# Kernel optimization log

Measured on AMD Instinct MI355X. Metric: run time of the kernel, lower is better.

Reference implementation:

```python
import jax, jax.numpy as jnp
import numpy as np

NHEAD = 16
NEG1 = -9e15   # first masked_fill value (-9000000000000000.0)
NEG2 = -9e16   # second masked_fill value


def setup_inputs() -> dict:
    key = jax.random.key(0)
    ks = jax.random.split(key, 8)
    slen, bsz, emb = 512, 16, 1024
    x = jax.random.normal(ks[0], (slen, bsz, emb), dtype=jnp.float32)
    mask = jax.random.randint(ks[1], (bsz, slen, slen), 0, 2, dtype=jnp.int32)
    weight_mask = jax.random.randint(ks[2], (bsz, slen, slen), 0, 2, dtype=jnp.int32)
    s = 1.0 / np.sqrt(emb)
    Wq = jax.random.normal(ks[3], (emb, emb), dtype=jnp.float32) * s
    Wk = jax.random.normal(ks[4], (emb, emb), dtype=jnp.float32) * s
    Wv = jax.random.normal(ks[5], (emb, emb), dtype=jnp.float32) * s
    Ws = jax.random.normal(ks[6], (emb, emb), dtype=jnp.float32) * s
    Wb = jax.random.normal(ks[7], (1, 3 * emb), dtype=jnp.float32) * s
    return {"x": x, "mask": mask, "weight_mask": weight_mask,
            "Wq": Wq, "Wk": Wk, "Wv": Wv, "Ws": Ws, "Wb": Wb}


def reference(x, mask, weight_mask, Wq, Wk, Wv, Ws, Wb):
    slen, bsz, emb = x.shape
    hd = emb // NHEAD
    scaling = float(hd) ** -0.5

    def split_heads(t):  # (slen, bsz, emb) -> (bsz, nhead, slen, hd)
        return t.reshape(slen, bsz, NHEAD, hd).transpose(1, 2, 0, 3)

    q = split_heads(x @ Wq.T)
    k = split_heads(x @ Wk.T)
    v = split_heads(x @ Wv.T)

    attn = jnp.einsum('bhqd,bhkd->bhqk', q, k) * scaling

    m = mask.astype(attn.dtype)[:, None, :, :]          # (bsz,1,slen,slen)
    attn = jnp.where(m == 0, NEG1, attn)
    attn = jax.nn.softmax(attn, axis=-1) * m

    wm = weight_mask.astype(attn.dtype)[:, None, :, :]
    attn = jnp.where(wm == 0, NEG2, attn)
    attn = jax.nn.softmax(attn, axis=-1) * wm
    # degree normalization: row-normalize
    attn = attn * (1.0 / (attn.sum(-1) + 1e-10))[..., None]

    # dropout inactive (eval mode)
    out = jnp.einsum('bhqk,bhkd->bhqd', attn, v)         # (bsz,nhead,slen,hd)
    out = out.transpose(2, 0, 1, 3).reshape(slen, bsz, emb)

    r = x @ Ws.T
    gate = jax.nn.sigmoid(jnp.concatenate([out, r, out - r], axis=-1) @ Wb.T)
    return gate * r + (1.0 - gate) * out
```

## Files before the change

kernel.cpp:

```cpp
#include <hip/hip_runtime.h>
#include <hip/hip_bf16.h>
#include <stdint.h>

typedef __attribute__((ext_vector_type(8))) short short8;
typedef __attribute__((ext_vector_type(4))) float f32x4;
typedef __attribute__((ext_vector_type(4))) unsigned short ushort4v;

#define MFMA_BF16(a,b,c) __builtin_amdgcn_mfma_f32_16x16x32_bf16((a),(b),(c),0,0,0)

static __device__ __forceinline__ unsigned short f2bf(float f){
  union { float fv; unsigned int u; } c; c.fv = f;
  unsigned int u = c.u;
  return (unsigned short)((u + 0x7fffu + ((u >> 16) & 1u)) >> 16);
}

static __device__ __forceinline__ unsigned int cvtpk(float a, float b){
  unsigned int r;
  asm("v_cvt_pk_bf16_f32 %0, %1, %2" : "=v"(r) : "v"(a), "v"(b));
  return r;
}

static __device__ __forceinline__ void gload_lds16(const void* g, void* l){
  __builtin_amdgcn_global_load_lds(
      (const __attribute__((address_space(1))) void*)g,
      (__attribute__((address_space(3))) void*)l, 16, 0, 0);
}

static __device__ __forceinline__ float wred_sum(float v){
  #pragma unroll
  for (int m = 32; m; m >>= 1) v += __shfl_xor(v, m, 64);
  return v;
}

static __device__ __forceinline__ void unpack8(uint4 u, float* f){
  f[0] = __uint_as_float(u.x << 16); f[1] = __uint_as_float(u.x & 0xFFFF0000u);
  f[2] = __uint_as_float(u.y << 16); f[3] = __uint_as_float(u.y & 0xFFFF0000u);
  f[4] = __uint_as_float(u.z << 16); f[5] = __uint_as_float(u.z & 0xFFFF0000u);
  f[6] = __uint_as_float(u.w << 16); f[7] = __uint_as_float(u.w & 0xFFFF0000u);
}

__global__ __launch_bounds__(256) void cvt_x_kernel(const float* __restrict__ x,
                                                    unsigned short* __restrict__ o){
  int i = blockIdx.x * 256 + threadIdx.x;
  float4 f = ((const float4*)x)[i];
  ushort4v r;
  r[0] = f2bf(f.x); r[1] = f2bf(f.y); r[2] = f2bf(f.z); r[3] = f2bf(f.w);
  ((ushort4v*)o)[i] = r;
}

__global__ __launch_bounds__(256) void cvt_w_kernel(const float* __restrict__ Wq,
                                                    const float* __restrict__ Wk,
                                                    const float* __restrict__ Wv,
                                                    const float* __restrict__ Ws,
                                                    unsigned short* __restrict__ B){
  int i = blockIdx.x * 256 + threadIdx.x;
  int which = i >> 18;
  const float* src = (which == 0) ? Wq : (which == 1) ? Wk : (which == 2) ? Wv : Ws;
  float4 f = ((const float4*)src)[i & 262143];
  ushort4v r;
  r[0] = f2bf(f.x); r[1] = f2bf(f.y); r[2] = f2bf(f.z); r[3] = f2bf(f.w);
  ((ushort4v*)B)[i] = r;
}

__global__ void wb_prep_kernel(const float* __restrict__ Wb,
                               float* __restrict__ wba, float* __restrict__ wbb){
  int e = blockIdx.x * 256 + threadIdx.x;
  if (e < 1024){
    wba[e] = Wb[e]        + Wb[2048 + e];
    wbb[e] = Wb[1024 + e] - Wb[2048 + e];
  }
}

__global__ __launch_bounds__(256) void mask_prep_kernel(
    const int* __restrict__ m, const int* __restrict__ wm,
    unsigned long long* __restrict__ mb, unsigned long long* __restrict__ wb)
{
  const size_t i = (size_t)blockIdx.x * 256 + threadIdx.x;
  const int a = m[i];
  const int c = wm[i];
  unsigned long long ba = __ballot(a != 0);
  unsigned long long bc = __ballot(c != 0);
  if ((threadIdx.x & 63) == 0){
    mb[i >> 6] = ba;
    wb[i >> 6] = bc;
  }
}

__global__ __launch_bounds__(256, 4) void gemm_proj_kernel(
    const unsigned short* __restrict__ X, const unsigned short* __restrict__ B,
    unsigned short* __restrict__ qb, unsigned short* __restrict__ kb,
    unsigned short* __restrict__ vT, unsigned short* __restrict__ rbb)
{
  __shared__ __align__(16) unsigned short smem[128 * 136];
  unsigned short* As = smem;
  unsigned short* Bs = smem + 4096;
  const int tid = threadIdx.x;
  const int w = tid >> 6, l = tid & 63;
  const int lr = l & 15, lq = l >> 4;
  const int wr = w >> 1, wc = w & 1;
  const int bid = ((blockIdx.x & 7) << 8) | (blockIdx.x >> 3);
  const int m0 = (bid >> 5) * 128;
  const int n0 = (bid & 31) * 128;
  const int gsw = (lr >> 1) & 3;
  f32x4 acc[4][4] = {};

  for (int k0 = 0; k0 < 1024; k0 += 32){
    #pragma unroll
    for (int i = 0; i < 2; i++){
      const int c = i * 256 + tid;
      const int row = c >> 2;
      const int cgs = (c & 3) ^ ((c >> 3) & 3);
      gload_lds16(X + (size_t)(m0 + row) * 1024 + k0 + cgs * 8,
                  As + (i * 256 + w * 64) * 8);
      gload_lds16(B + (size_t)(n0 + row) * 1024 + k0 + cgs * 8,
                  Bs + (i * 256 + w * 64) * 8);
    }
    __syncthreads();
    short8 av[4], bv[4];
    #pragma unroll
    for (int mf = 0; mf < 4; mf++)
      av[mf] = *(const short8*)(As + (wr * 64 + mf * 16 + lr) * 32 + (lq ^ gsw) * 8);
    #pragma unroll
    for (int nf = 0; nf < 4; nf++)
      bv[nf] = *(const short8*)(Bs + (wc * 64 + nf * 16 + lr) * 32 + (lq ^ gsw) * 8);
    #pragma unroll
    for (int mf = 0; mf < 4; mf++)
      #pragma unroll
      for (int nf = 0; nf < 4; nf++)
        acc[mf][nf] = MFMA_BF16(av[mf], bv[nf], acc[mf][nf]);
    __syncthreads();
  }

  const int which = (n0 >> 10);
  const int o0 = n0 & 1023;
  if (which == 2){
    #pragma unroll
    for (int mf = 0; mf < 4; mf++)
      #pragma unroll
      for (int nf = 0; nf < 4; nf++){
        const int r0 = wr * 64 + mf * 16 + lq * 4;
        const int c  = wc * 64 + nf * 16 + lr;
        uint2 pk;
        pk.x = cvtpk(acc[mf][nf][0], acc[mf][nf][1]);
        pk.y = cvtpk(acc[mf][nf][2], acc[mf][nf][3]);
        *(uint2*)(smem + c * 132 + r0) = pk;
      }
    __syncthreads();
    const int s0 = m0 >> 4;
    #pragma unroll
    for (int p = 0; p < 8; p++){
      const int cid = p * 256 + tid;
      const int c = cid >> 4, bb = cid & 15;
      short8 st;
      #pragma unroll
      for (int j = 0; j < 8; j++) st[j] = (short)smem[c * 132 + j * 16 + bb];
      const int o = o0 + c;
      const int bh = bb * 16 + (o >> 6), d = o & 63;
      *(short8*)(vT + ((size_t)bh * 64 + d) * 512 + s0) = st;
    }
  } else {
    #pragma unroll
    for (int mf = 0; mf < 4; mf++)
      #pragma unroll
      for (int nf = 0; nf < 4; nf++)
        #pragma unroll
        for (int rg = 0; rg < 4; rg++)
          smem[(wr * 64 + mf * 16 + lq * 4 + rg) * 136 + wc * 64 + nf * 16 + lr]
              = f2bf(acc[mf][nf][rg]);
    __syncthreads();
    if (which == 3){
      #pragma unroll
      for (int p = 0; p < 8; p++){
        const int cid = p * 256 + tid;
        const int lrow = cid >> 4, cg = cid & 15;
        short8 vv = *(const short8*)(smem + lrow * 136 + cg * 8);
        *(short8*)(rbb + (size_t)(m0 + lrow) * 1024 + o0 + cg * 8) = vv;
      }
    } else {
      unsigned short* dst = (which == 0) ? qb : kb;
      #pragma unroll
      for (int p = 0; p < 8; p++){
        const int cid = p * 256 + tid;
        const int lrow = cid >> 4, cg = cid & 15;
        short8 vv = *(const short8*)(smem + lrow * 136 + cg * 8);
        const int rowi = m0 + lrow;
        const int s = rowi >> 4, bb = rowi & 15;
        const int o = o0 + cg * 8;
        const int bh = bb * 16 + (o >> 6), d = o & 63;
        *(short8*)(dst + ((size_t)bh * 512 + s) * 64 + d) = vv;
      }
    }
  }
}

__global__ __launch_bounds__(256, 4) void attn_kernel(
    const unsigned short* __restrict__ qg, const unsigned short* __restrict__ kg,
    const unsigned short* __restrict__ vt,
    const unsigned char* __restrict__ mbits, const unsigned char* __restrict__ wbits,
    unsigned short* __restrict__ outp)
{
  __shared__ __align__(16) unsigned short sE[32 * 520];
  __shared__ float sfin[32];
  const int bid = ((blockIdx.x & 7) << 9) | (blockIdx.x >> 3);
  const int qt = bid & 15, h = (bid >> 4) & 15, b = bid >> 8;
  const int tid = threadIdx.x, w = tid >> 6, l = tid & 63;
  const int lr = l & 15, lq = l >> 4;
  const int bh = b * 16 + h;
  const unsigned short* qp = qg + ((size_t)bh * 512 + qt * 32) * 64;
  const unsigned short* kp = kg + (size_t)bh * 512 * 64;
  const unsigned short* vp = vt + (size_t)bh * 64 * 512;

  const unsigned char* mrb = mbits + ((size_t)(b * 512 + qt * 32)) * 64;
  const unsigned char* wrb = wbits + ((size_t)(b * 512 + qt * 32)) * 64;
  unsigned int mby[2][4], wby[2][4];
  #pragma unroll
  for (int g = 0; g < 2; g++)
    #pragma unroll
    for (int rr = 0; rr < 4; rr++){
      mby[g][rr] = mrb[(g * 16 + w * 4 + rr) * 64 + l];
      wby[g][rr] = wrb[(g * 16 + w * 4 + rr) * 64 + l];
    }

  short8 qa[2][2];
  #pragma unroll
  for (int t = 0; t < 2; t++){
    qa[t][0] = *(const short8*)(qp + (t * 16 + lr) * 64 + lq * 8);
    qa[t][1] = *(const short8*)(qp + (t * 16 + lr) * 64 + 32 + lq * 8);
  }
  const float CEXP = 0.18033688011112042f;
  #pragma unroll
  for (int kf = 0; kf < 8; kf++){
    const unsigned short* kr = kp + (size_t)(w * 128 + kf * 16 + lr) * 64;
    short8 k0 = *(const short8*)(kr + lq * 8);
    short8 k1 = *(const short8*)(kr + 32 + lq * 8);
    f32x4 a0 = {}, a1 = {};
    a0 = MFMA_BF16(qa[0][0], k0, a0);
    a1 = MFMA_BF16(qa[1][0], k0, a1);
    a0 = MFMA_BF16(qa[0][1], k1, a0);
    a1 = MFMA_BF16(qa[1][1], k1, a1);
    const int col = w * 128 + kf * 16 + lr;
    #pragma unroll
    for (int t = 0; t < 2; t++){
      f32x4 a = t ? a1 : a0;
      float e0 = __builtin_amdgcn_exp2f(a[0] * CEXP);
      float e1 = __builtin_amdgcn_exp2f(a[1] * CEXP);
      float e2 = __builtin_amdgcn_exp2f(a[2] * CEXP);
      float e3 = __builtin_amdgcn_exp2f(a[3] * CEXP);
      unsigned int p01 = cvtpk(e0, e1), p23 = cvtpk(e2, e3);
      const int row = t * 16 + lq * 4;
      sE[(row    ) * 520 + col] = (unsigned short)(p01 & 0xFFFFu);
      sE[(row + 1) * 520 + col] = (unsigned short)(p01 >> 16);
      sE[(row + 2) * 520 + col] = (unsigned short)(p23 & 0xFFFFu);
      sE[(row + 3) * 520 + col] = (unsigned short)(p23 >> 16);
    }
  }
  __syncthreads();

  #pragma unroll
  for (int g = 0; g < 2; g++){
    const int row0 = g * 16 + w * 4;
    uint4 ev[4];
    #pragma unroll
    for (int rr = 0; rr < 4; rr++)
      ev[rr] = *(const uint4*)(sE + (row0 + rr) * 520 + l * 8);

    float em[4][8]; float z1[4];
    #pragma unroll
    for (int rr = 0; rr < 4; rr++){
      float e1[8];
      unpack8(ev[rr], e1);
      const unsigned int mb = mby[g][rr];
      float z = 0.f;
      #pragma unroll
      for (int j = 0; j < 8; j++){
        em[rr][j] = ((mb >> j) & 1u) ? e1[j] : 0.f;
        z += em[rr][j];
      }
      z1[rr] = z;
    }
    #pragma unroll
    for (int m = 32; m; m >>= 1){
      #pragma unroll
      for (int rr = 0; rr < 4; rr++) z1[rr] += __shfl_xor(z1[rr], m, 64);
    }
    float e2[4][8]; float z2[4];
    #pragma unroll
    for (int rr = 0; rr < 4; rr++){
      const float i1L = 1.4426950408889634f / z1[rr];
      const unsigned int wv = wby[g][rr];
      float z = 0.f;
      #pragma unroll
      for (int j = 0; j < 8; j++){
        float t = __builtin_amdgcn_exp2f(em[rr][j] * i1L);
        e2[rr][j] = ((wv >> j) & 1u) ? t : 0.f;
        z += e2[rr][j];
      }
      z2[rr] = z;
    }
    #pragma unroll
    for (int m = 32; m; m >>= 1){
      #pragma unroll
      for (int rr = 0; rr < 4; rr++) z2[rr] += __shfl_xor(z2[rr], m, 64);
    }
    #pragma unroll
    for (int rr = 0; rr < 4; rr++){
      uint4 o;
      o.x = cvtpk(e2[rr][0], e2[rr][1]); o.y = cvtpk(e2[rr][2], e2[rr][3]);
      o.z = cvtpk(e2[rr][4], e2[rr][5]); o.w = cvtpk(e2[rr][6], e2[rr][7]);
      *(uint4*)(sE + (row0 + rr) * 520 + l * 8) = o;
      if (l == 0) sfin[row0 + rr] = 1.f / (z2[rr] + 1e-10f);
    }
  }
  __syncthreads();

  {
    f32x4 po0 = {}, po1 = {};
    #pragma unroll
    for (int ks = 0; ks < 16; ks++){
      short8 vf = *(const short8*)(vp + (size_t)(w * 16 + lr) * 512 + ks * 32 + lq * 8);
      short8 af0 = *(const short8*)(sE + (     lr) * 520 + ks * 32 + lq * 8);
      short8 af1 = *(const short8*)(sE + (16 + lr) * 520 + ks * 32 + lq * 8);
      po0 = MFMA_BF16(af0, vf, po0);
      po1 = MFMA_BF16(af1, vf, po1);
    }
    #pragma unroll
    for (int rg = 0; rg < 4; rg++){
      const int r0 = lq * 4 + rg;
      outp[((size_t)(qt * 32 + r0) * 16 + b) * 1024 + h * 64 + w * 16 + lr]
          = f2bf(po0[rg] * sfin[r0]);
      outp[((size_t)(qt * 32 + 16 + r0) * 16 + b) * 1024 + h * 64 + w * 16 + lr]
          = f2bf(po1[rg] * sfin[16 + r0]);
    }
  }
}

__global__ __launch_bounds__(256) void gate_kernel(
    const unsigned short* __restrict__ outp, const unsigned short* __restrict__ rbb,
    const float* __restrict__ wba, const float* __restrict__ wbb,
    float* __restrict__ y)
{
  const int t = blockIdx.x * 4 + (threadIdx.x >> 6);
  const int l = threadIdx.x & 63;
  const unsigned short* o = outp + (size_t)t * 1024;
  const unsigned short* r = rbb + (size_t)t * 1024;
  float ov[16], rv[16];
  float acc = 0.f;
  #pragma unroll
  for (int j = 0; j < 16; j++){
    const int e = j * 64 + l;
    ov[j] = __uint_as_float((unsigned int)o[e] << 16);
    rv[j] = __uint_as_float((unsigned int)r[e] << 16);
    acc += ov[j] * wba[e] + rv[j] * wbb[e];
  }
  const float dot = wred_sum(acc);
  const float g = 1.f / (1.f + __builtin_amdgcn_exp2f(-dot * 1.4426950408889634f));
  float* yo = y + (size_t)t * 1024;
  #pragma unroll
  for (int j = 0; j < 16; j++){
    const int e = j * 64 + l;
    yo[e] = g * rv[j] + (1.f - g) * ov[j];
  }
}

extern "C" void kernel_launch(void* const* d_in, const int* in_sizes, int n_in,
                              void* d_out, int out_size, void* d_ws, size_t ws_size,
                              hipStream_t stream)
{
  (void)in_sizes; (void)n_in; (void)out_size; (void)ws_size;
  const float* x   = (const float*)d_in[0];
  const int* mask  = (const int*)d_in[1];
  const int* wmask = (const int*)d_in[2];
  const float* Wq  = (const float*)d_in[3];
  const float* Wk  = (const float*)d_in[4];
  const float* Wv  = (const float*)d_in[5];
  const float* Ws  = (const float*)d_in[6];
  const float* Wb  = (const float*)d_in[7];

  char* ws = (char*)d_ws;
  unsigned short* xbf = (unsigned short*)ws; ws += 16777216;
  unsigned short* bm  = (unsigned short*)ws; ws += 8388608;
  unsigned short* qb  = (unsigned short*)ws; ws += 16777216;
  unsigned short* kb  = (unsigned short*)ws; ws += 16777216;
  unsigned short* vT  = (unsigned short*)ws; ws += 16777216;
  unsigned short* rbb = (unsigned short*)ws; ws += 16777216;
  unsigned short* op  = (unsigned short*)ws; ws += 16777216;
  float* wba = (float*)ws; ws += 4096;
  float* wbb = (float*)ws; ws += 4096;
  unsigned long long* mb64 = (unsigned long long*)xbf;
  unsigned long long* wb64 = (unsigned long long*)bm;

  cvt_x_kernel<<<8192, 256, 0, stream>>>(x, xbf);
  cvt_w_kernel<<<4096, 256, 0, stream>>>(Wq, Wk, Wv, Ws, bm);
  wb_prep_kernel<<<4, 256, 0, stream>>>(Wb, wba, wbb);
  gemm_proj_kernel<<<2048, 256, 0, stream>>>(xbf, bm, qb, kb, vT, rbb);
  mask_prep_kernel<<<16384, 256, 0, stream>>>(mask, wmask, mb64, wb64);
  attn_kernel<<<4096, 256, 0, stream>>>(qb, kb, vT,
      (const unsigned char*)mb64, (const unsigned char*)wb64, op);
  gate_kernel<<<2048, 256, 0, stream>>>(op, rbb, wba, wbb, (float*)d_out);
}
```

Baseline: 201.8 us.

## Restructure projection GEMM into 256x128 tiles with triple-buffered async LDS pipeline

Rewrites the QKV/S projection GEMM to use 512-thread blocks computing 256x128 tiles with a K-step of 64. Loads go through a three-stage LDS ring buffer with vmcnt-based waits, so the next tiles are fetched while the MFMAs run, and MFMA sections get raised scheduling priority. It also changes the XOR swizzle and splits the epilogue into two halves to fit LDS. The cost targeted is global-load latency exposed by the old single-buffered, barrier-heavy loop. In exchange it uses 144KB of LDS, which allows only one block per CU and lowers occupancy.

After: 185.4 us. 1.09x faster.

```diff
diff --git a/kernel.cpp b/kernel.cpp
--- a/kernel.cpp
+++ b/kernel.cpp
@@ -86,111 +86,143 @@
   }
 }
 
-__global__ __launch_bounds__(256, 4) void gemm_proj_kernel(
+__global__ __launch_bounds__(512, 1) void gemm_proj_kernel(
     const unsigned short* __restrict__ X, const unsigned short* __restrict__ B,
     unsigned short* __restrict__ qb, unsigned short* __restrict__ kb,
     unsigned short* __restrict__ vT, unsigned short* __restrict__ rbb)
 {
-  __shared__ __align__(16) unsigned short smem[128 * 136];
-  unsigned short* As = smem;
-  unsigned short* Bs = smem + 4096;
+  __shared__ __align__(16) unsigned short smem[73728];
   const int tid = threadIdx.x;
   const int w = tid >> 6, l = tid & 63;
   const int lr = l & 15, lq = l >> 4;
-  const int wr = w >> 1, wc = w & 1;
-  const int bid = ((blockIdx.x & 7) << 8) | (blockIdx.x >> 3);
-  const int m0 = (bid >> 5) * 128;
-  const int n0 = (bid & 31) * 128;
-  const int gsw = (lr >> 1) & 3;
+  const int wm = w >> 1, wn = w & 1;
+  const int bid = ((blockIdx.x & 7) << 7) | (blockIdx.x >> 3);
+  const int mt = bid >> 5, nt = bid & 31;
+  const int m0 = mt * 256, n0 = nt * 128;
+  const int lrow8 = l >> 3, lc = l & 7;
+
   f32x4 acc[4][4] = {};
 
-  for (int k0 = 0; k0 < 1024; k0 += 32){
-    #pragma unroll
-    for (int i = 0; i < 2; i++){
-      const int c = i * 256 + tid;
-      const int row = c >> 2;
-      const int cgs = (c & 3) ^ ((c >> 3) & 3);
-      gload_lds16(X + (size_t)(m0 + row) * 1024 + k0 + cgs * 8,
-                  As + (i * 256 + w * 64) * 8);
-      gload_lds16(B + (size_t)(n0 + row) * 1024 + k0 + cgs * 8,
-                  Bs + (i * 256 + w * 64) * 8);
-    }
+  #define STAGE(T) { \
+    const int bufo_ = ((T) % 3) * 24576; \
+    const int kk_ = (T) * 64; \
+    _Pragma("unroll") \
+    for (int j = 0; j < 4; j++){ \
+      const int seg = w + j * 8; \
+      const int r = seg * 8 + lrow8; \
+      gload_lds16(X + (size_t)(m0 + r) * 1024 + kk_ + ((lc ^ (r & 7)) * 8), \
+                  smem + bufo_ + seg * 512); \
+    } \
+    _Pragma("unroll") \
+    for (int j = 0; j < 2; j++){ \
+      const int seg = w + j * 8; \
+      const int r = seg * 8 + lrow8; \
+      gload_lds16(B + (size_t)(n0 + r) * 1024 + kk_ + ((lc ^ (r & 7)) * 8), \
+                  smem + bufo_ + 16384 + seg * 512); \
+    } }
+
+  #define COMPUTE(T) { \
+    const int bo_ = ((T) % 3) * 24576; \
+    _Pragma("unroll") \
+    for (int subk = 0; subk < 2; subk++){ \
+      short8 av[4], bv[4]; \
+      const int pc = (((subk * 4 + lq) ^ (lr & 7)) * 8); \
+      _Pragma("unroll") \
+      for (int mf = 0; mf < 4; mf++) \
+        av[mf] = *(const short8*)(smem + bo_ + (wm * 64 + mf * 16 + lr) * 64 + pc); \
+      _Pragma("unroll") \
+      for (int nf = 0; nf < 4; nf++) \
+        bv[nf] = *(const short8*)(smem + bo_ + 16384 + (wn * 64 + nf * 16 + lr) * 64 + pc); \
+      __builtin_amdgcn_s_setprio(1); \
+      _Pragma("unroll") \
+      for (int mf = 0; mf < 4; mf++) \
+        _Pragma("unroll") \
+        for (int nf = 0; nf < 4; nf++) \
+          acc[mf][nf] = MFMA_BF16(av[mf], bv[nf], acc[mf][nf]); \
+      __builtin_amdgcn_s_setprio(0); \
+    } }
+
+  STAGE(0)
+  STAGE(1)
+
+  for (int t = 0; t < 15; t++){
+    asm volatile("s_waitcnt vmcnt(6)" ::: "memory");
+    __builtin_amdgcn_s_barrier();
+    if (t < 14) STAGE(t + 2)
+    COMPUTE(t)
+  }
+  asm volatile("s_waitcnt vmcnt(0)" ::: "memory");
+  __builtin_amdgcn_s_barrier();
+  COMPUTE(15)
+
+  const int which = nt >> 3;
+  const int o0 = (nt & 7) * 128;
+  if (which == 2){
     __syncthreads();
-    short8 av[4], bv[4];
     #pragma unroll
     for (int mf = 0; mf < 4; mf++)
-      av[mf] = *(const short8*)(As + (wr * 64 + mf * 16 + lr) * 32 + (lq ^ gsw) * 8);
-    #pragma unroll
-    for (int nf = 0; nf < 4; nf++)
-      bv[nf] = *(const short8*)(Bs + (wc * 64 + nf * 16 + lr) * 32 + (lq ^ gsw) * 8);
-    #pragma unroll
-    for (int mf = 0; mf < 4; mf++)
-      #pragma unroll
-      for (int nf = 0; nf < 4; nf++)
-        acc[mf][nf] = MFMA_BF16(av[mf], bv[nf], acc[mf][nf]);
-    __syncthreads();
-  }
-
-  const int which = (n0 >> 10);
-  const int o0 = n0 & 1023;
-  if (which == 2){
-    #pragma unroll
-    for (int mf = 0; mf < 4; mf++)
       #pragma unroll
       for (int nf = 0; nf < 4; nf++){
-        const int r0 = wr * 64 + mf * 16 + lq * 4;
-        const int c  = wc * 64 + nf * 16 + lr;
+        const int c = wn * 64 + nf * 16 + lr;
+        const int r0v = wm * 64 + mf * 16 + lq * 4;
         uint2 pk;
         pk.x = cvtpk(acc[mf][nf][0], acc[mf][nf][1]);
         pk.y = cvtpk(acc[mf][nf][2], acc[mf][nf][3]);
-        *(uint2*)(smem + c * 132 + r0) = pk;
+        *(uint2*)(smem + c * 264 + r0v) = pk;
       }
     __syncthreads();
-    const int s0 = m0 >> 4;
     #pragma unroll
     for (int p = 0; p < 8; p++){
-      const int cid = p * 256 + tid;
-      const int c = cid >> 4, bb = cid & 15;
+      const int cid = p * 512 + tid;
+      const int c = cid >> 5, bb = (cid >> 1) & 15, sh = cid & 1;
       short8 st;
       #pragma unroll
-      for (int j = 0; j < 8; j++) st[j] = (short)smem[c * 132 + j * 16 + bb];
+      for (int j = 0; j < 8; j++) st[j] = (short)smem[c * 264 + (sh * 8 + j) * 16 + bb];
       const int o = o0 + c;
       const int bh = bb * 16 + (o >> 6), d = o & 63;
-      *(short8*)(vT + ((size_t)bh * 64 + d) * 512 + s0) = st;
+      *(short8*)(vT + ((size_t)bh * 64 + d) * 512 + mt * 16 + sh * 8) = st;
     }
   } else {
     #pragma unroll
-    for (int mf = 0; mf < 4; mf++)
-      #pragma unroll
-      for (int nf = 0; nf < 4; nf++)
+    for (int h2 = 0; h2 < 2; h2++){
+      __syncthreads();
+      if ((wm >> 1) == h2){
         #pragma unroll
-        for (int rg = 0; rg < 4; rg++)
-          smem[(wr * 64 + mf * 16 + lq * 4 + rg) * 136 + wc * 64 + nf * 16 + lr]
-              = f2bf(acc[mf][nf][rg]);
-    __syncthreads();
-    if (which == 3){
-      #pragma unroll
-      for (int p = 0; p < 8; p++){
-        const int cid = p * 256 + tid;
-        const int lrow = cid >> 4, cg = cid & 15;
-        short8 vv = *(const short8*)(smem + lrow * 136 + cg * 8);
-        *(short8*)(rbb + (size_t)(m0 + lrow) * 1024 + o0 + cg * 8) = vv;
+        for (int mf = 0; mf < 4; mf++)
+          #pragma unroll
+          for (int nf = 0; nf < 4; nf++)
+            #pragma unroll
+            for (int rg = 0; rg < 4; rg++)
+              smem[((wm & 1) * 64 + mf * 16 + lq * 4 + rg) * 136 + wn * 64 + nf * 16 + lr]
+                  = f2bf(acc[mf][nf][rg]);
       }
-    } else {
-      unsigned short* dst = (which == 0) ? qb : kb;
-      #pragma unroll
-      for (int p = 0; p < 8; p++){
-        const int cid = p * 256 + tid;
-        const int lrow = cid >> 4, cg = cid & 15;
-        short8 vv = *(const short8*)(smem + lrow * 136 + cg * 8);
-        const int rowi = m0 + lrow;
-        const int s = rowi >> 4, bb = rowi & 15;
-        const int o = o0 + cg * 8;
-        const int bh = bb * 16 + (o >> 6), d = o & 63;
-        *(short8*)(dst + ((size_t)bh * 512 + s) * 64 + d) = vv;
+      __syncthreads();
+      if (which == 3){
+        #pragma unroll
+        for (int p = 0; p < 4; p++){
+          const int cid = p * 512 + tid;
+          const int lrow = cid >> 4, cg = cid & 15;
+          short8 vv = *(const short8*)(smem + lrow * 136 + cg * 8);
+          *(short8*)(rbb + (size_t)(m0 + h2 * 128 + lrow) * 1024 + o0 + cg * 8) = vv;
+        }
+      } else {
+        unsigned short* dst = (which == 0) ? qb : kb;
+        #pragma unroll
+        for (int p = 0; p < 4; p++){
+          const int cid = p * 512 + tid;
+          const int lrow = cid >> 4, cg = cid & 15;
+          short8 vv = *(const short8*)(smem + lrow * 136 + cg * 8);
+          const int rowi = m0 + h2 * 128 + lrow;
+          const int s = rowi >> 4, bb = rowi & 15;
+          const int o = o0 + cg * 8;
+          const int bh = bb * 16 + (o >> 6), d = o & 63;
+          *(short8*)(dst + ((size_t)bh * 512 + s) * 64 + d) = vv;
+        }
       }
     }
   }
+  #undef STAGE
+  #undef COMPUTE
 }
 
 __global__ __launch_bounds__(256, 4) void attn_kernel(
@@ -392,7 +424,7 @@
   cvt_x_kernel<<<8192, 256, 0, stream>>>(x, xbf);
   cvt_w_kernel<<<4096, 256, 0, stream>>>(Wq, Wk, Wv, Ws, bm);
   wb_prep_kernel<<<4, 256, 0, stream>>>(Wb, wba, wbb);
-  gemm_proj_kernel<<<2048, 256, 0, stream>>>(xbf, bm, qb, kb, vT, rbb);
+  gemm_proj_kernel<<<1024, 512, 0, stream>>>(xbf, bm, qb, kb, vT, rbb);
   mask_prep_kernel<<<16384, 256, 0, stream>>>(mask, wmask, mb64, wb64);
   attn_kernel<<<4096, 256, 0, stream>>>(qb, kb, vT,
       (const unsigned char*)mb64, (const unsigned char*)wb64, op);
```
